# Optimization experiments

Hardware: AMD Instinct MI355X
Metric: run time of the kernel (lower is better)

The kernel has to match this reference:

```python
import jax, jax.numpy as jnp
import numpy as np

VOCAB, EMBD, H1, H2, OUT = 100000, 128, 256, 128, 1
EPS = 1e-12

def _layernorm(x, g, b):
    mu = jnp.mean(x, axis=-1, keepdims=True)
    var = jnp.mean(jnp.square(x - mu), axis=-1, keepdims=True)
    return (x - mu) * jax.lax.rsqrt(var + EPS) * g + b

def setup_inputs() -> dict:
    key = jax.random.key(0)
    ks = jax.random.split(key, 10)
    B, S = 4096, 50
    return {
        "entity_ids": jax.random.randint(ks[0], (B, S), 0, VOCAB),
        "entity_length": jax.random.randint(ks[1], (B,), 0, S + 1),
        "emb_table": jax.random.normal(ks[2], (VOCAB, EMBD), jnp.float32),
        "ln1_g": jnp.ones((EMBD,), jnp.float32),
        "ln1_b": jnp.zeros((EMBD,), jnp.float32),
        "w1": jax.random.normal(ks[3], (EMBD, H1), jnp.float32) * (1.0 / np.sqrt(EMBD)),
        "b1": jnp.zeros((H1,), jnp.float32),
        "w2": jax.random.normal(ks[4], (H1, H2), jnp.float32) * (1.0 / np.sqrt(H1)),
        "b2": jnp.zeros((H2,), jnp.float32),
        "ln2_g": jnp.ones((H2,), jnp.float32),
        "ln2_b": jnp.zeros((H2,), jnp.float32),
        "fc_w": jax.random.normal(ks[5], (H2, OUT), jnp.float32) * (1.0 / np.sqrt(H2)),
        "fc_b": jnp.zeros((OUT,), jnp.float32),
    }

def reference(entity_ids, entity_length, emb_table, ln1_g, ln1_b, w1, b1, w2, b2, ln2_g, ln2_b, fc_w, fc_b):
    # embed: [B, S, EMBD]
    x = emb_table[entity_ids]
    x = _layernorm(x, ln1_g, ln1_b)
    # MLP (dropout is identity in eval); torch GELU default is exact erf form
    x = jax.nn.gelu(x @ w1 + b1, approximate=False) @ w2 + b2  # [B, S, H2]
    # ragged max-pool over first length positions (length 0 treated as 1)
    lengths = jnp.maximum(entity_length, 1)  # [B]
    S = x.shape[1]
    mask = jnp.arange(S)[None, :] < lengths[:, None]  # [B, S]
    x = jnp.max(jnp.where(mask[:, :, None], x, -jnp.inf), axis=1)  # [B, H2]
    x = _layernorm(x, ln2_g, ln2_b)
    return (x @ fc_w + fc_b).squeeze(-1)  # [B]
```

## Files before the change

kernel.cpp:

```cpp
#include <hip/hip_runtime.h>
#include <hip/hip_bf16.h>
#include <math.h>

typedef __attribute__((ext_vector_type(8))) _Float16 half8;
typedef __attribute__((ext_vector_type(4))) _Float16 half4;
typedef __attribute__((ext_vector_type(4))) float f32x4;

#define EMBD 128
#define H1 256
#define H2 128
#define SLEN 50
#define NROWS 4096
#define MTILE 32
#define DENSE_GRID 512

#define WS_FRAGS    0
#define WS_CNT      131072
#define WS_ROWSTART 131200
#define WS_PACKED   147584
#define WS_PARTIAL  966784

__device__ __forceinline__ float gelu_exact(float h) {
    float ah = fabsf(h);
    float d  = fmaf(0.23163845f, ah, 1.0f);
    float t;
    asm("v_rcp_f32 %0, %1" : "=v"(t) : "v"(d));
    float p = fmaf(1.061405429f, t, -1.453152027f);
    p = fmaf(p, t, 1.421413741f);
    p = fmaf(p, t, -0.284496736f);
    p = fmaf(p, t, 0.254829592f);
    p = p * t;
    float e;
    float x2 = h * h * -0.72134752f;
    asm("v_exp_f32 %0, %1" : "=v"(e) : "v"(x2));
    float er = fmaf(-p, e, 1.0f);
    return fmaf(0.5f * ah, er, 0.5f * h);
}

#define BARRIER_LDS() asm volatile("s_waitcnt lgkmcnt(0)\n\ts_barrier" ::: "memory")

__global__ __launch_bounds__(256) void setup_kernel(
    const float* __restrict__ w1, const float* __restrict__ w2,
    const int* __restrict__ ids, const int* __restrict__ lens,
    half8* __restrict__ frags, unsigned* __restrict__ packed,
    int* __restrict__ cnt, int* __restrict__ rowstart)
{
    int b = blockIdx.x, t = threadIdx.x;
    if (b < 32) {
        int f = b * 256 + t;
        half8 v;
        if (f < 4096) {
            int fragid = f >> 6, lane = f & 63;
            int kt = fragid >> 4, nt = fragid & 15;
            int col = nt * 16 + (lane & 15);
            int kb  = kt * 32 + (lane >> 4) * 8;
            #pragma unroll
            for (int i = 0; i < 8; ++i) v[i] = (_Float16)w1[(size_t)(kb + i) * H1 + col];
            frags[f] = v;
        } else {
            int f2 = f - 4096;
            int fragid = f2 >> 6, lane = f2 & 63;
            int kt = fragid >> 3, ntc = fragid & 7;
            int col = ntc * 16 + (lane & 15);
            int kb  = kt * 32 + (lane >> 4) * 8;
            #pragma unroll
            for (int i = 0; i < 8; ++i) v[i] = (_Float16)w2[(size_t)(kb + i) * H2 + col];
            frags[4096 + f2] = v;
        }
    } else {
        int gtid = (b - 32) * 256 + t;
        int lane = t & 63;
        int len = lens[gtid]; len = len < 1 ? 1 : (len > SLEN ? SLEN : len);
        int inc = len;
        #pragma unroll
        for (int off = 1; off < 64; off <<= 1) {
            int v = __shfl_up(inc, off, 64);
            if (lane >= off) inc += v;
        }
        int wave_total = __shfl(inc, 63, 64);
        int wbase;
        if (lane == 0) wbase = atomicAdd(cnt, wave_total);
        wbase = __shfl(wbase, 0, 64);
        int base = wbase + inc - len;
        rowstart[gtid] = base;
        unsigned rtag = (unsigned)gtid << 17;
        for (int k = 0; k < len; ++k)
            packed[base + k] = (unsigned)ids[gtid * SLEN + k] | rtag;
    }
}

__global__ __launch_bounds__(512) void dense_kernel(
    const unsigned* __restrict__ packed, const int* __restrict__ cnt,
    const float* __restrict__ emb, const float* __restrict__ ln1g,
    const float* __restrict__ ln1b, const float* __restrict__ b1,
    const float* __restrict__ b2, const half8* __restrict__ wfrag,
    float* __restrict__ partial)
{
    const int tid = threadIdx.x;
    const int w  = tid >> 6;
    const int l  = tid & 63;
    const int ln = l & 15;
    const int lg = l >> 4;
    const int g32 = w * 4 + lg;

    __shared__ __align__(16) _Float16 x_lds[MTILE][EMBD + 8];
    __shared__ __align__(16) _Float16 h1_lds[MTILE][H1 + 8];
    __shared__ unsigned tok_lds[MTILE + 1];
    __shared__ __align__(16) float b1s[H1];
    __shared__ float b2s[H2];

    if (tid < H1) b1s[tid] = b1[tid];
    else if (tid < H1 + H2) b2s[tid - H1] = b2[tid - H1];

    half8 w1r[4][2];
    #pragma unroll
    for (int kt = 0; kt < 4; ++kt)
      #pragma unroll
      for (int j = 0; j < 2; ++j)
        w1r[kt][j] = wfrag[(kt * 16 + w * 2 + j) * 64 + l];
    half8 w2r[8];
    #pragma unroll
    for (int kt = 0; kt < 8; ++kt)
        w2r[kt] = wfrag[4096 + (kt * 8 + w) * 64 + l];

    float g1r[8], b1r[8];
    #pragma unroll
    for (int i = 0; i < 8; ++i) { g1r[i] = ln1g[ln * 8 + i]; b1r[i] = ln1b[ln * 8 + i]; }

    const int total = *cnt;

    int tile = blockIdx.x;
    int base = tile * MTILE;

    unsigned pkA = 0xFFFFFFFFu, tokA = 0xFFFFFFFFu;
    float4 pa0, pa1; bool vA = false;
    if (base < total) {
        if (base + g32 < total) pkA = packed[base + g32];
        if (tid <= 32) {
            int ti = (tid < 32) ? base + tid : base - 1;
            tokA = (ti >= 0 && ti < total) ? packed[ti] : 0xFFFFFFFFu;
        }
        vA = (pkA != 0xFFFFFFFFu);
        if (vA) {
            const float4* src = (const float4*)(emb + (size_t)(pkA & 0x1FFFFu) * EMBD + ln * 8);
            pa0 = src[0]; pa1 = src[1];
        }
    }

    for (; base < total; tile += (int)gridDim.x, base = tile * MTILE) {
        const int nbase = (tile + (int)gridDim.x) * MTILE;

        if (tid <= 32) tok_lds[tid] = tokA;

        unsigned pkN = 0xFFFFFFFFu, tokN = 0xFFFFFFFFu;
        if (nbase < total) {
            if (nbase + g32 < total) pkN = packed[nbase + g32];
            if (tid <= 32) {
                int ti = (tid < 32) ? nbase + tid : nbase - 1;
                tokN = (ti < total) ? packed[ti] : 0xFFFFFFFFu;
            }
        }

        {
            half8 xo;
            if (vA) {
                float v[8] = {pa0.x, pa0.y, pa0.z, pa0.w, pa1.x, pa1.y, pa1.z, pa1.w};
                float sm = 0.f, ss = 0.f;
                #pragma unroll
                for (int k = 0; k < 8; ++k) { sm += v[k]; ss += v[k] * v[k]; }
                #pragma unroll
                for (int m = 1; m < 16; m <<= 1) {
                    sm += __shfl_xor(sm, m, 64);
                    ss += __shfl_xor(ss, m, 64);
                }
                float mu  = sm * (1.f / 128.f);
                float var = ss * (1.f / 128.f) - mu * mu;
                float rs  = rsqrtf(var + 1e-12f);
                #pragma unroll
                for (int k = 0; k < 8; ++k)
                    xo[k] = (_Float16)((v[k] - mu) * rs * g1r[k] + b1r[k]);
            } else {
                #pragma unroll
                for (int k = 0; k < 8; ++k) xo[k] = (_Float16)0.f;
            }
            *(half8*)&x_lds[g32][ln * 8] = xo;
        }

        BARRIER_LDS();

        f32x4 acc[2][2];
        acc[0][0] = (f32x4){0,0,0,0}; acc[0][1] = (f32x4){0,0,0,0};
        acc[1][0] = (f32x4){0,0,0,0}; acc[1][1] = (f32x4){0,0,0,0};
        #pragma unroll
        for (int kt = 0; kt < 4; ++kt) {
            half8 xf0 = *(const half8*)&x_lds[ln][kt * 32 + lg * 8];
            half8 xf1 = *(const half8*)&x_lds[16 + ln][kt * 32 + lg * 8];
            acc[0][0] = __builtin_amdgcn_mfma_f32_16x16x32_f16(w1r[kt][0], xf0, acc[0][0], 0, 0, 0);
            acc[0][1] = __builtin_amdgcn_mfma_f32_16x16x32_f16(w1r[kt][1], xf0, acc[0][1], 0, 0, 0);
            acc[1][0] = __builtin_amdgcn_mfma_f32_16x16x32_f16(w1r[kt][0], xf1, acc[1][0], 0, 0, 0);
            acc[1][1] = __builtin_amdgcn_mfma_f32_16x16x32_f16(w1r[kt][1], xf1, acc[1][1], 0, 0, 0);
        }

        float4 pb0, pb1; bool vN = (pkN != 0xFFFFFFFFu);
        if (vN) {
            const float4* src = (const float4*)(emb + (size_t)(pkN & 0x1FFFFu) * EMBD + ln * 8);
            pb0 = src[0]; pb1 = src[1];
        }

        #pragma unroll
        for (int m = 0; m < 2; ++m)
          #pragma unroll
          for (int j = 0; j < 2; ++j) {
            f32x4 bb = *(const f32x4*)&b1s[(w * 2 + j) * 16 + lg * 4];
            half4 hv;
            #pragma unroll
            for (int g2 = 0; g2 < 4; ++g2) {
                float h = acc[m][j][g2] + bb[g2];
                hv[g2] = (_Float16)gelu_exact(h);
            }
            *(half4*)&h1_lds[m * 16 + ln][(w * 2 + j) * 16 + lg * 4] = hv;
          }

        int rowj = 0x7FFF, rowp = 0x7FFF;
        if (l < 32) {
            rowj = (int)(tok_lds[l] >> 17);
            rowp = (l == 0) ? (int)(tok_lds[32] >> 17) : (int)(tok_lds[l - 1] >> 17);
        }
        const int prevrow = (int)(tok_lds[32] >> 17);
        bool st = (l < 32) && ((l == 0) || (rowj != rowp));
        unsigned mask = (unsigned)__ballot(st);
        const float b2v = b2s[w * 16 + ln];

        BARRIER_LDS();

        f32x4 acc2[2];
        acc2[0] = (f32x4){0,0,0,0}; acc2[1] = (f32x4){0,0,0,0};
        #pragma unroll
        for (int kt = 0; kt < 8; ++kt) {
            half8 a0 = *(const half8*)&h1_lds[ln][kt * 32 + lg * 8];
            half8 a1 = *(const half8*)&h1_lds[16 + ln][kt * 32 + lg * 8];
            acc2[0] = __builtin_amdgcn_mfma_f32_16x16x32_f16(a0, w2r[kt], acc2[0], 0, 0, 0);
            acc2[1] = __builtin_amdgcn_mfma_f32_16x16x32_f16(a1, w2r[kt], acc2[1], 0, 0, 0);
        }
        float val[2][4];
        #pragma unroll
        for (int m = 0; m < 2; ++m)
          #pragma unroll
          for (int g2 = 0; g2 < 4; ++g2)
            val[m][g2] = acc2[m][g2] + b2v;

        {
            int s0 = 0;
            while (s0 < 32) {
                int s1;
                if (s0 >= 31) s1 = 32;
                else {
                    unsigned m2 = mask >> (s0 + 1);
                    s1 = m2 ? (s0 + __ffs(m2)) : 32;
                }
                int row = __shfl(rowj, s0, 64);
                if (row < NROWS) {
                    float mx = -INFINITY;
                    #pragma unroll
                    for (int m = 0; m < 2; ++m)
                      #pragma unroll
                      for (int g2 = 0; g2 < 4; ++g2) {
                        int tt = m * 16 + lg * 4 + g2;
                        if (tt >= s0 && tt < s1) mx = fmaxf(mx, val[m][g2]);
                      }
                    mx = fmaxf(mx, __shfl_xor(mx, 16, 64));
                    mx = fmaxf(mx, __shfl_xor(mx, 32, 64));
                    int side = (s0 == 0 && row == prevrow) ? 1 + (tile & 1) : 0;
                    if (l < 16)
                        partial[(size_t)row * 384 + side * 128 + w * 16 + l] = mx;
                }
                s0 = s1;
            }
        }

        pkA = pkN; tokA = tokN; vA = vN;
        if (vN) { pa0 = pb0; pa1 = pb1; }
    }
}

__global__ __launch_bounds__(256) void head_kernel(
    const float* __restrict__ partial, const int* __restrict__ rowstart,
    const int* __restrict__ lens, const float* __restrict__ ln2g,
    const float* __restrict__ ln2b, const float* __restrict__ fcw,
    const float* __restrict__ fcb, float* __restrict__ out)
{
    int w = threadIdx.x >> 6, l = threadIdx.x & 63;
    int r = blockIdx.x * 4 + w;
    const float* pr = partial + (size_t)r * 384;

    int start = rowstart[r];
    int len = lens[r]; len = len < 1 ? 1 : (len > SLEN ? SLEN : len);
    int tf = start >> 5, tl = (start + len - 1) >> 5;

    float v0 = pr[l], v1 = pr[64 + l];
    if (tl > tf) {
        int side = 1 + ((tf + 1) & 1);
        v0 = fmaxf(v0, pr[side * 128 + l]);
        v1 = fmaxf(v1, pr[side * 128 + 64 + l]);
    }
    if (tl > tf + 1) {
        int side = 1 + ((tf + 2) & 1);
        v0 = fmaxf(v0, pr[side * 128 + l]);
        v1 = fmaxf(v1, pr[side * 128 + 64 + l]);
    }

    float g2a = ln2g[l], g2c = ln2g[l + 64];
    float b2a = ln2b[l], b2c = ln2b[l + 64];
    float fwa = fcw[l],  fwc = fcw[l + 64];
    float s = v0 + v1, ss = v0 * v0 + v1 * v1;
    #pragma unroll
    for (int m = 1; m < 64; m <<= 1) {
        s  += __shfl_xor(s,  m, 64);
        ss += __shfl_xor(ss, m, 64);
    }
    float mu  = s * (1.f / 128.f);
    float var = ss * (1.f / 128.f) - mu * mu;
    float rs  = rsqrtf(var + 1e-12f);
    float n0 = (v0 - mu) * rs * g2a + b2a;
    float n1 = (v1 - mu) * rs * g2c + b2c;
    float dot = n0 * fwa + n1 * fwc;
    #pragma unroll
    for (int m = 1; m < 64; m <<= 1) dot += __shfl_xor(dot, m, 64);
    if (l == 0) out[r] = dot + fcb[0];
}

extern "C" void kernel_launch(void* const* d_in, const int* in_sizes, int n_in,
                              void* d_out, int out_size, void* d_ws, size_t ws_size,
                              hipStream_t stream) {
    const int*   ids  = (const int*)d_in[0];
    const int*   lens = (const int*)d_in[1];
    const float* emb  = (const float*)d_in[2];
    const float* ln1g = (const float*)d_in[3];
    const float* ln1b = (const float*)d_in[4];
    const float* w1   = (const float*)d_in[5];
    const float* b1   = (const float*)d_in[6];
    const float* w2   = (const float*)d_in[7];
    const float* b2   = (const float*)d_in[8];
    const float* ln2g = (const float*)d_in[9];
    const float* ln2b = (const float*)d_in[10];
    const float* fcw  = (const float*)d_in[11];
    const float* fcb  = (const float*)d_in[12];
    float* out = (float*)d_out;

    char* ws = (char*)d_ws;
    half8*    frags    = (half8*)(ws + WS_FRAGS);
    int*      cnt      = (int*)(ws + WS_CNT);
    int*      rowstart = (int*)(ws + WS_ROWSTART);
    unsigned* packed   = (unsigned*)(ws + WS_PACKED);
    float*    partial  = (float*)(ws + WS_PARTIAL);

    hipMemsetAsync(cnt, 0, sizeof(int), stream);
    hipLaunchKernelGGL(setup_kernel, dim3(48), dim3(256), 0, stream,
                       w1, w2, ids, lens, frags, packed, cnt, rowstart);
    hipLaunchKernelGGL(dense_kernel, dim3(DENSE_GRID), dim3(512), 0, stream,
                       packed, cnt, emb, ln1g, ln1b, b1, b2, frags, partial);
    hipLaunchKernelGGL(head_kernel, dim3(1024), dim3(256), 0, stream,
                       partial, rowstart, lens, ln2g, ln2b, fcw, fcb, out);
}
```

Baseline: 72.31 us.

## Replace atomic row packing with deterministic prefix sums; drop memset, enlarge dense grid

```diff
diff --git a/kernel.cpp b/kernel.cpp
--- a/kernel.cpp
+++ b/kernel.cpp
@@ -12,13 +12,12 @@
 #define SLEN 50
 #define NROWS 4096
 #define MTILE 32
-#define DENSE_GRID 512
+#define DENSE_GRID 768
 
 #define WS_FRAGS    0
-#define WS_CNT      131072
-#define WS_ROWSTART 131200
-#define WS_PACKED   147584
-#define WS_PARTIAL  966784
+#define WS_ROWSTART 131072
+#define WS_PACKED   147456
+#define WS_PARTIAL  966656
 
 __device__ __forceinline__ float gelu_exact(float h) {
     float ah = fabsf(h);
@@ -39,11 +38,15 @@
 
 #define BARRIER_LDS() asm volatile("s_waitcnt lgkmcnt(0)\n\ts_barrier" ::: "memory")
 
+__device__ __forceinline__ int clamp_len(int v) {
+    return v < 1 ? 1 : (v > SLEN ? SLEN : v);
+}
+
 __global__ __launch_bounds__(256) void setup_kernel(
     const float* __restrict__ w1, const float* __restrict__ w2,
     const int* __restrict__ ids, const int* __restrict__ lens,
     half8* __restrict__ frags, unsigned* __restrict__ packed,
-    int* __restrict__ cnt, int* __restrict__ rowstart)
+    int* __restrict__ rowstart)
 {
     int b = blockIdx.x, t = threadIdx.x;
     if (b < 32) {
@@ -68,29 +71,34 @@
             frags[4096 + f2] = v;
         }
     } else {
-        int gtid = (b - 32) * 256 + t;
         int lane = t & 63;
-        int len = lens[gtid]; len = len < 1 ? 1 : (len > SLEN ? SLEN : len);
+        int wv   = t >> 6;
+        int start_row = ((b - 32) * 4 + wv) * 64;
+
+        int acc = 0;
+        for (int j = lane; j < start_row; j += 64) acc += clamp_len(lens[j]);
+        #pragma unroll
+        for (int m = 1; m < 64; m <<= 1) acc += __shfl_xor(acc, m, 64);
+
+        int r   = start_row + lane;
+        int len = clamp_len(lens[r]);
         int inc = len;
         #pragma unroll
         for (int off = 1; off < 64; off <<= 1) {
             int v = __shfl_up(inc, off, 64);
             if (lane >= off) inc += v;
         }
-        int wave_total = __shfl(inc, 63, 64);
-        int wbase;
-        if (lane == 0) wbase = atomicAdd(cnt, wave_total);
-        wbase = __shfl(wbase, 0, 64);
-        int base = wbase + inc - len;
-        rowstart[gtid] = base;
-        unsigned rtag = (unsigned)gtid << 17;
+        int base = acc + inc - len;
+        rowstart[r] = base;
+        unsigned rtag = (unsigned)r << 17;
         for (int k = 0; k < len; ++k)
-            packed[base + k] = (unsigned)ids[gtid * SLEN + k] | rtag;
+            packed[base + k] = (unsigned)ids[r * SLEN + k] | rtag;
     }
 }
 
 __global__ __launch_bounds__(512) void dense_kernel(
-    const unsigned* __restrict__ packed, const int* __restrict__ cnt,
+    const unsigned* __restrict__ packed, const int* __restrict__ rowstart,
+    const int* __restrict__ lens,
     const float* __restrict__ emb, const float* __restrict__ ln1g,
     const float* __restrict__ ln1b, const float* __restrict__ b1,
     const float* __restrict__ b2, const half8* __restrict__ wfrag,
@@ -127,7 +135,9 @@
     #pragma unroll
     for (int i = 0; i < 8; ++i) { g1r[i] = ln1g[ln * 8 + i]; b1r[i] = ln1b[ln * 8 + i]; }
 
-    const int total = *cnt;
+    int lastLen = lens[NROWS - 1];
+    lastLen = lastLen < 1 ? 1 : (lastLen > SLEN ? SLEN : lastLen);
+    const int total = rowstart[NROWS - 1] + lastLen;
 
     int tile = blockIdx.x;
     int base = tile * MTILE;
@@ -349,16 +359,14 @@
 
     char* ws = (char*)d_ws;
     half8*    frags    = (half8*)(ws + WS_FRAGS);
-    int*      cnt      = (int*)(ws + WS_CNT);
     int*      rowstart = (int*)(ws + WS_ROWSTART);
     unsigned* packed   = (unsigned*)(ws + WS_PACKED);
     float*    partial  = (float*)(ws + WS_PARTIAL);
 
-    hipMemsetAsync(cnt, 0, sizeof(int), stream);
     hipLaunchKernelGGL(setup_kernel, dim3(48), dim3(256), 0, stream,
-                       w1, w2, ids, lens, frags, packed, cnt, rowstart);
+                       w1, w2, ids, lens, frags, packed, rowstart);
     hipLaunchKernelGGL(dense_kernel, dim3(DENSE_GRID), dim3(512), 0, stream,
-                       packed, cnt, emb, ln1g, ln1b, b1, b2, frags, partial);
+                       packed, rowstart, lens, emb, ln1g, ln1b, b1, b2, frags, partial);
     hipLaunchKernelGGL(head_kernel, dim3(1024), dim3(256), 0, stream,
                        partial, rowstart, lens, ln2g, ln2b, fcw, fcb, out);
 }
```

Result: no change. 70.92 us (-1.9%).
